# Performance work log

Measured on AMD Instinct MI355X. Metric: run time of the kernel, lower is better.

The kernel has to match this reference:

```python
import jax, jax.numpy as jnp
import numpy as np

N = 8192          # total samples = n_ways * num_instances
D = 512           # embedding dim
NUM_INSTANCES = 8 # shots per class
MARGIN = 0.3
W = 1.0
EPS = 1e-12


def setup_inputs() -> dict:
    key = jax.random.key(0)
    inputs = jax.random.normal(key, (N, D), dtype=jnp.float32)
    # targets[i] = class id; classes are contiguous blocks of NUM_INSTANCES
    targets = jnp.arange(N, dtype=jnp.int32) // NUM_INSTANCES
    return {"inputs": inputs, "targets": targets}


def _pairwise_euclid(a, b):
    # sqrt(clamp(||a||^2 + ||b||^2 - 2 a.b, eps)) -- same as torch addmm path
    sq_a = jnp.sum(a * a, axis=1)          # [na]
    sq_b = jnp.sum(b * b, axis=1)          # [nb]
    d2 = sq_a[:, None] + sq_b[None, :] - 2.0 * (a @ b.T)
    return jnp.sqrt(jnp.clip(d2, EPS, None))


def reference(inputs, targets):
    n = inputs.shape[0]
    n_ways = n // NUM_INSTANCES

    dist = _pairwise_euclid(inputs, inputs)              # [n, n]
    mask = targets[:, None] == targets[None, :]          # same-class mask

    # batch-hard mining: hardest positive (max same-class dist),
    # hardest negative (min different-class dist), fully vectorized
    dist_ap = jnp.max(jnp.where(mask, dist, -jnp.inf), axis=1)  # [n]
    dist_an = jnp.min(jnp.where(mask, jnp.inf, dist), axis=1)   # [n]

    # MarginRankingLoss with y=1: mean(relu(-(dist_an - dist_ap) + margin))
    loss = jnp.mean(jax.nn.relu(dist_ap - dist_an + MARGIN))

    dist_p = jnp.mean(dist_ap)
    dist_n = jnp.mean(dist_an)

    # prototype accuracy
    protos = inputs.reshape(n_ways, NUM_INSTANCES, -1).mean(axis=1)  # [n_ways, D]
    logits = _pairwise_euclid(inputs, protos)                        # [n, n_ways]
    estimate = jnp.argmin(logits, axis=1)
    labels = jnp.arange(n_ways, dtype=estimate.dtype).repeat(NUM_INSTANCES)
    acc = jnp.mean((estimate == labels).astype(jnp.float32))

    return (W * loss, acc, dist_p, dist_n)
```

## Files before the change

### kernel.cpp

```cpp
#include <hip/hip_runtime.h>
#include <hip/hip_bf16.h>
#include <stdint.h>

#define NTOT  8192
#define DIM   512
#define NI    8
#define NWAYS 1024
#define TILE  128
#define BK    64
#define NSYM  2080
#define NBLK  2592
#define MARGINV 0.3f

typedef float f32x4 __attribute__((ext_vector_type(4)));

__device__ __forceinline__ unsigned f2o(float f) {
  unsigned u = __float_as_uint(f);
  return (u & 0x80000000u) ? ~u : (u | 0x80000000u);
}
__device__ __forceinline__ float o2f(unsigned u) {
  u = (u & 0x80000000u) ? (u & 0x7fffffffu) : ~u;
  return __uint_as_float(u);
}

__device__ __forceinline__ float wave_sum64(float v) {
#pragma unroll
  for (int s = 32; s; s >>= 1) v += __shfl_xor(v, s, 64);
  return v;
}

__device__ __forceinline__ void async_ld16(const void* g, void* l) {
  __builtin_amdgcn_global_load_lds(
      (__attribute__((address_space(1))) void*)(uintptr_t)g,
      (__attribute__((address_space(3))) void*)l, 16, 0, 0);
}

__global__ __launch_bounds__(256) void prep(
    const float* __restrict__ A, float* __restrict__ sq,
    float* __restrict__ psq, unsigned char* __restrict__ A8,
    unsigned char* __restrict__ P8,
    unsigned* __restrict__ an_u32, unsigned* __restrict__ ap_u32,
    unsigned long long* __restrict__ pr_key) {
  const int w = threadIdx.x >> 6;
  const int l = threadIdx.x & 63;
  const int b = blockIdx.x;
  if (b < NTOT / 4) {
    const int row = b * 4 + w;
    const float4* rp = (const float4*)(A + (size_t)row * DIM);
    unsigned* op = (unsigned*)(A8 + (size_t)row * DIM);
    float s = 0.f;
#pragma unroll
    for (int m = 0; m < 2; ++m) {
      const float4 v = rp[l + 64 * m];
      s = fmaf(v.x, v.x, fmaf(v.y, v.y, fmaf(v.z, v.z, fmaf(v.w, v.w, s))));
      int wd = 0;
      wd = __builtin_amdgcn_cvt_pk_fp8_f32(v.x, v.y, wd, false);
      wd = __builtin_amdgcn_cvt_pk_fp8_f32(v.z, v.w, wd, true);
      op[l + 64 * m] = (unsigned)wd;
    }
    s = wave_sum64(s);
    if (l == 0) {
      sq[row] = s;
      an_u32[row] = ~0u;
      ap_u32[row] = 0u;
      pr_key[row] = ~0ull;
    }
  } else {
    const int c = (b - NTOT / 4) * 4 + w;
    unsigned* op = (unsigned*)(P8 + (size_t)c * DIM);
    float s = 0.f;
#pragma unroll
    for (int m = 0; m < 2; ++m) {
      float4 p = {0.f, 0.f, 0.f, 0.f};
#pragma unroll
      for (int r = 0; r < NI; ++r) {
        const float4 v =
            ((const float4*)(A + (size_t)(c * NI + r) * DIM))[l + 64 * m];
        p.x += v.x; p.y += v.y; p.z += v.z; p.w += v.w;
      }
      p.x *= (1.f / NI); p.y *= (1.f / NI); p.z *= (1.f / NI); p.w *= (1.f / NI);
      s = fmaf(p.x, p.x, fmaf(p.y, p.y, fmaf(p.z, p.z, fmaf(p.w, p.w, s))));
      int wd = 0;
      wd = __builtin_amdgcn_cvt_pk_fp8_f32(p.x, p.y, wd, false);
      wd = __builtin_amdgcn_cvt_pk_fp8_f32(p.z, p.w, wd, true);
      op[l + 64 * m] = (unsigned)wd;
    }
    s = wave_sum64(s);
    if (l == 0) psq[c] = s;
  }
}

__global__ __launch_bounds__(256) void gemm_fused(
    const unsigned char* __restrict__ A, const unsigned char* __restrict__ P,
    const float* __restrict__ sq, const float* __restrict__ psq,
    unsigned* __restrict__ an_u32, unsigned* __restrict__ ap_u32,
    unsigned long long* __restrict__ pr_key) {
  __shared__ __align__(16) unsigned char As[2][TILE * BK];
  __shared__ __align__(16) unsigned char Bs[2][TILE * BK];
  __shared__ unsigned rmin[TILE];
  __shared__ unsigned cmin[TILE];
  __shared__ unsigned amax[TILE];
  __shared__ unsigned long long rowkey[TILE][2];

  const int braw = blockIdx.x;
  const int b = (braw & 7) * (NBLK / 8) + (braw >> 3);
  const bool isProto = b >= NSYM;
  int bi, bj;
  const unsigned char* Bmat;
  const float* sqB;
  if (!isProto) {
    int rem = b, Si = 0, Sj = 0;
    for (;;) {
      const int cnt = (Si == Sj) ? 36 : 64;
      if (rem < cnt) break;
      rem -= cnt;
      ++Si;
      if (Si > Sj) { Si = 0; ++Sj; }
    }
    int bi_l, bj_l;
    if (Si == Sj) {
      bj_l = 0;
      while ((bj_l + 1) * (bj_l + 2) / 2 <= rem) ++bj_l;
      bi_l = rem - bj_l * (bj_l + 1) / 2;
    } else {
      bi_l = rem & 7;
      bj_l = rem >> 3;
    }
    bi = Si * 8 + bi_l;
    bj = Sj * 8 + bj_l;
    Bmat = A;
    sqB = sq;
  } else {
    const int p = b - NSYM;
    bj = p & 7;
    bi = p >> 3;
    Bmat = P;
    sqB = psq;
  }
  const int rowBase = bi * TILE;
  const int colBase = bj * TILE;
  const bool isDiag = !isProto && (bi == bj);
  const bool colSide = !isProto && (bi != bj);

  const int t = threadIdx.x;
  const int lane = t & 63;
  const int wv = t >> 6;
  const int wr = wv >> 1;
  const int wc = wv & 1;
  const int quad = lane >> 4;
  const int lc = lane & 15;

  if (t < TILE) { rmin[t] = ~0u; cmin[t] = ~0u; amax[t] = 0u; }

  const int kf = (lc ^ (lc >> 2)) & 3;
  int koff[2];
#pragma unroll
  for (int c = 0; c < 2; ++c)
    koff[c] = (((c * 2 + (quad >> 1)) ^ kf) * 16) + (quad & 1) * 8;

  int rowA[4], rowB[4];
#pragma unroll
  for (int x = 0; x < 4; ++x) {
    rowA[x] = (wr * 64 + x * 16 + lc) * BK;
    rowB[x] = (wc * 64 + x * 16 + lc) * BK;
  }

  const int l4 = lane >> 2;
  const int ul = ((lane & 3) ^ ((l4 ^ (l4 >> 2)) & 3)) * 16;
  const unsigned char* gA = A + (size_t)(rowBase + l4) * DIM + ul;
  const unsigned char* gB = Bmat + (size_t)(colBase + l4) * DIM + ul;
  const int ldsL = lane * 16;

  f32x4 acc[4][4] = {};

#pragma unroll
  for (int j = 0; j < 2; ++j) {
    const int rr = wv * 2 + j;
    async_ld16(gA + (size_t)rr * 16 * DIM, &As[0][rr * 1024 + ldsL]);
    async_ld16(gB + (size_t)rr * 16 * DIM, &Bs[0][rr * 1024 + ldsL]);
  }
  __syncthreads();

#pragma unroll
  for (int it = 0; it < 8; ++it) {
    const int cur = it & 1;
    const int nxt = cur ^ 1;
    const int kt = it * BK;
    if (it < 7) {
#pragma unroll
      for (int j = 0; j < 2; ++j) {
        const int rr = wv * 2 + j;
        async_ld16(gA + (size_t)rr * 16 * DIM + kt + BK, &As[nxt][rr * 1024 + ldsL]);
        async_ld16(gB + (size_t)rr * 16 * DIM + kt + BK, &Bs[nxt][rr * 1024 + ldsL]);
      }
    }
    const unsigned char* Ac = &As[cur][0];
    const unsigned char* Bc = &Bs[cur][0];
#pragma unroll
    for (int c = 0; c < 2; ++c) {
      long af[4], bfr[4];
#pragma unroll
      for (int x = 0; x < 4; ++x) {
        af[x]  = *(const long*)(Ac + rowA[x] + koff[c]);
        bfr[x] = *(const long*)(Bc + rowB[x] + koff[c]);
      }
#pragma unroll
      for (int x = 0; x < 4; ++x)
#pragma unroll
        for (int y = 0; y < 4; ++y)
          acc[x][y] = __builtin_amdgcn_mfma_f32_16x16x32_fp8_fp8(
              af[x], bfr[y], acc[x][y], 0, 0, 0);
    }
    __syncthreads();
  }

  float sb[4];
#pragma unroll
  for (int y = 0; y < 4; ++y) sb[y] = sqB[colBase + wc * 64 + y * 16 + lc];

  const float INF = __int_as_float(0x7f800000);

  if (!isProto) {
#pragma unroll
    for (int x = 0; x < 4; ++x) {
#pragma unroll
      for (int r = 0; r < 4; ++r) {
        const int row = rowBase + wr * 64 + x * 16 + quad * 4 + r;
        float mv = INF, mx = -INF;
#pragma unroll
        for (int y = 0; y < 4; ++y) {
          const float v = fmaf(-2.f, acc[x][y][r], sb[y]);
          if (isDiag) {
            const int col = colBase + wc * 64 + y * 16 + lc;
            const bool same = (row >> 3) == (col >> 3);
            mv = fminf(mv, same ? INF : v);
            mx = fmaxf(mx, same ? v : -INF);
          } else {
            mv = fminf(mv, v);
          }
        }
#pragma unroll
        for (int s = 1; s < 16; s <<= 1) {
          mv = fminf(mv, __shfl_xor(mv, s, 64));
          if (isDiag) mx = fmaxf(mx, __shfl_xor(mx, s, 64));
        }
        if (lc == 0) {
          atomicMin(&rmin[row - rowBase], f2o(mv));
          if (isDiag) atomicMax(&amax[row - rowBase], f2o(mx));
        }
      }
    }
    if (colSide) {
      float sa[4][4];
#pragma unroll
      for (int x = 0; x < 4; ++x)
#pragma unroll
        for (int r = 0; r < 4; ++r)
          sa[x][r] = sq[rowBase + wr * 64 + x * 16 + quad * 4 + r];
#pragma unroll
      for (int y = 0; y < 4; ++y) {
        float cv = INF;
#pragma unroll
        for (int x = 0; x < 4; ++x)
#pragma unroll
          for (int r = 0; r < 4; ++r)
            cv = fminf(cv, fmaf(-2.f, acc[x][y][r], sa[x][r]));
        cv = fminf(cv, __shfl_xor(cv, 16, 64));
        cv = fminf(cv, __shfl_xor(cv, 32, 64));
        if (quad == 0) atomicMin(&cmin[wc * 64 + y * 16 + lc], f2o(cv));
      }
    }
  } else {
#pragma unroll
    for (int x = 0; x < 4; ++x) {
      unsigned long long kmin[4] = {~0ull, ~0ull, ~0ull, ~0ull};
#pragma unroll
      for (int y = 0; y < 4; ++y) {
        const int col = colBase + wc * 64 + y * 16 + lc;
#pragma unroll
        for (int r = 0; r < 4; ++r) {
          const float v = fmaf(-2.f, acc[x][y][r], sb[y]);
          const unsigned long long kn =
              ((unsigned long long)f2o(v) << 32) | (unsigned)col;
          if (kn < kmin[r]) kmin[r] = kn;
        }
      }
#pragma unroll
      for (int r = 0; r < 4; ++r) {
#pragma unroll
        for (int s = 1; s < 16; s <<= 1) {
          const unsigned long long o = __shfl_xor(kmin[r], s, 64);
          if (o < kmin[r]) kmin[r] = o;
        }
      }
      if (lc == 0) {
#pragma unroll
        for (int r = 0; r < 4; ++r)
          rowkey[wr * 64 + x * 16 + quad * 4 + r][wc] = kmin[r];
      }
    }
  }

  __syncthreads();
  if (isProto) {
    if (t < TILE) {
      unsigned long long a = rowkey[t][0];
      const unsigned long long c = rowkey[t][1];
      if (c < a) a = c;
      atomicMin(pr_key + rowBase + t, a);
    }
  } else {
    if (t < TILE) {
      atomicMin(an_u32 + rowBase + t, rmin[t]);
    } else if (t < 2 * TILE) {
      const int i = t - TILE;
      if (colSide) atomicMin(an_u32 + colBase + i, cmin[i]);
      else if (isDiag) atomicMax(ap_u32 + rowBase + i, amax[i]);
    }
  }
}

__global__ void finalize_kernel(const float* __restrict__ sq,
                                const unsigned* __restrict__ an_u32,
                                const unsigned* __restrict__ ap_u32,
                                const unsigned long long* __restrict__ pr_key,
                                float* __restrict__ out) {
  const int tid = threadIdx.x;
  float loss = 0.f, sp = 0.f, sn = 0.f, acc = 0.f;
#pragma unroll
  for (int i = tid; i < NTOT; i += 1024) {
    const float s = sq[i];
    const float ap = sqrtf(fmaxf(s + o2f(ap_u32[i]), 1e-12f));
    const float an = sqrtf(fmaxf(s + o2f(an_u32[i]), 1e-12f));
    loss += fmaxf(ap - an + MARGINV, 0.f);
    sp += ap;
    sn += an;
    acc += ((unsigned)(pr_key[i] & 0xffffffffu) == (unsigned)(i >> 3)) ? 1.f : 0.f;
  }
  loss = wave_sum64(loss);
  sp = wave_sum64(sp);
  sn = wave_sum64(sn);
  acc = wave_sum64(acc);
  __shared__ float red[16][4];
  const int w = tid >> 6, l = tid & 63;
  if (l == 0) { red[w][0] = loss; red[w][1] = acc; red[w][2] = sp; red[w][3] = sn; }
  __syncthreads();
  if (tid == 0) {
    float L = 0, Ac = 0, Pm = 0, Nn = 0;
    for (int i = 0; i < 16; ++i) {
      L += red[i][0]; Ac += red[i][1]; Pm += red[i][2]; Nn += red[i][3];
    }
    out[0] = L / NTOT;
    out[1] = Ac / NTOT;
    out[2] = Pm / NTOT;
    out[3] = Nn / NTOT;
  }
}

extern "C" void kernel_launch(void* const* d_in, const int* in_sizes, int n_in,
                              void* d_out, int out_size, void* d_ws, size_t ws_size,
                              hipStream_t stream) {
  const float* inputs = (const float*)d_in[0];
  float* out = (float*)d_out;
  char* w = (char*)d_ws;
  float* sq  = (float*)(w);
  float* psq = (float*)(w + 32768);
  unsigned* an_u32 = (unsigned*)(w + 36864);
  unsigned* ap_u32 = (unsigned*)(w + 69632);
  unsigned long long* pr_key = (unsigned long long*)(w + 102400);
  unsigned char* A8 = (unsigned char*)(w + 167936);
  unsigned char* P8 = (unsigned char*)(w + 167936 + (size_t)NTOT * DIM);

  prep<<<NTOT / 4 + NWAYS / 4, 256, 0, stream>>>(inputs, sq, psq, A8, P8,
                                                 an_u32, ap_u32, pr_key);
  gemm_fused<<<NBLK, 256, 0, stream>>>(A8, P8, sq, psq,
                                       an_u32, ap_u32, pr_key);
  finalize_kernel<<<1, 1024, 0, stream>>>(sq, an_u32, ap_u32, pr_key, out);
}
```

Baseline: 149.4 us.

## Triple-buffer LDS tiles with vmcnt-based waits, hoist norm loads, raise MFMA priority

Replaces the double-buffered async global-to-LDS pipeline with a three-stage ring that prefetches two K-tiles ahead. It uses explicit s_waitcnt vmcnt plus s_barrier in place of __syncthreads, so one barrier per iteration covers both load completion and buffer reuse. The squared-norm loads for the epilogue are hoisted before the main loop so their latency overlaps the GEMM, and s_setprio raises wave priority around the MFMA bursts. The third buffer adds LDS per block, which may reduce occupancy. The hand-counted vmcnt values assume the hoisted sq loads retire early and that the issue order stays as written.

```diff
diff --git a/kernel.cpp b/kernel.cpp
--- a/kernel.cpp
+++ b/kernel.cpp
@@ -8,11 +8,15 @@
 #define NWAYS 1024
 #define TILE  128
 #define BK    64
+#define NBUF  3
 #define NSYM  2080
 #define NBLK  2592
 #define MARGINV 0.3f
 
 typedef float f32x4 __attribute__((ext_vector_type(4)));
+
+#define VMWAIT_BAR(N) \
+  asm volatile("s_waitcnt vmcnt(" #N ")\n\ts_barrier" ::: "memory")
 
 __device__ __forceinline__ unsigned f2o(float f) {
   unsigned u = __float_as_uint(f);
@@ -95,8 +99,8 @@
     const float* __restrict__ sq, const float* __restrict__ psq,
     unsigned* __restrict__ an_u32, unsigned* __restrict__ ap_u32,
     unsigned long long* __restrict__ pr_key) {
-  __shared__ __align__(16) unsigned char As[2][TILE * BK];
-  __shared__ __align__(16) unsigned char Bs[2][TILE * BK];
+  __shared__ __align__(16) unsigned char As[NBUF][TILE * BK];
+  __shared__ __align__(16) unsigned char Bs[NBUF][TILE * BK];
   __shared__ unsigned rmin[TILE];
   __shared__ unsigned cmin[TILE];
   __shared__ unsigned amax[TILE];
@@ -152,6 +156,19 @@
 
   if (t < TILE) { rmin[t] = ~0u; cmin[t] = ~0u; amax[t] = 0u; }
 
+  float sb[4];
+#pragma unroll
+  for (int y = 0; y < 4; ++y) sb[y] = sqB[colBase + wc * 64 + y * 16 + lc];
+  float sa[4][4];
+  if (colSide) {
+#pragma unroll
+    for (int x = 0; x < 4; ++x)
+#pragma unroll
+      for (int r = 0; r < 4; ++r)
+        sa[x][r] = sq[rowBase + wr * 64 + x * 16 + quad * 4 + r];
+  }
+  asm volatile("" ::: "memory");
+
   const int kf = (lc ^ (lc >> 2)) & 3;
   int koff[2];
 #pragma unroll
@@ -174,28 +191,31 @@
   f32x4 acc[4][4] = {};
 
 #pragma unroll
-  for (int j = 0; j < 2; ++j) {
-    const int rr = wv * 2 + j;
-    async_ld16(gA + (size_t)rr * 16 * DIM, &As[0][rr * 1024 + ldsL]);
-    async_ld16(gB + (size_t)rr * 16 * DIM, &Bs[0][rr * 1024 + ldsL]);
-  }
-  __syncthreads();
+  for (int tt = 0; tt < 2; ++tt) {
+#pragma unroll
+    for (int j = 0; j < 2; ++j) {
+      const int rr = wv * 2 + j;
+      async_ld16(gA + (size_t)rr * 16 * DIM + tt * BK, &As[tt][rr * 1024 + ldsL]);
+      async_ld16(gB + (size_t)rr * 16 * DIM + tt * BK, &Bs[tt][rr * 1024 + ldsL]);
+    }
+  }
 
 #pragma unroll
   for (int it = 0; it < 8; ++it) {
-    const int cur = it & 1;
-    const int nxt = cur ^ 1;
-    const int kt = it * BK;
-    if (it < 7) {
+    if (it < 7) VMWAIT_BAR(4);
+    else       VMWAIT_BAR(0);
+    if (it < 6) {
+      const int nb = (it + 2) % NBUF;
+      const int kt2 = (it + 2) * BK;
 #pragma unroll
       for (int j = 0; j < 2; ++j) {
         const int rr = wv * 2 + j;
-        async_ld16(gA + (size_t)rr * 16 * DIM + kt + BK, &As[nxt][rr * 1024 + ldsL]);
-        async_ld16(gB + (size_t)rr * 16 * DIM + kt + BK, &Bs[nxt][rr * 1024 + ldsL]);
-      }
-    }
-    const unsigned char* Ac = &As[cur][0];
-    const unsigned char* Bc = &Bs[cur][0];
+        async_ld16(gA + (size_t)rr * 16 * DIM + kt2, &As[nb][rr * 1024 + ldsL]);
+        async_ld16(gB + (size_t)rr * 16 * DIM + kt2, &Bs[nb][rr * 1024 + ldsL]);
+      }
+    }
+    const unsigned char* Ac = &As[it % NBUF][0];
+    const unsigned char* Bc = &Bs[it % NBUF][0];
 #pragma unroll
     for (int c = 0; c < 2; ++c) {
       long af[4], bfr[4];
@@ -204,19 +224,16 @@
         af[x]  = *(const long*)(Ac + rowA[x] + koff[c]);
         bfr[x] = *(const long*)(Bc + rowB[x] + koff[c]);
       }
+      __builtin_amdgcn_s_setprio(1);
 #pragma unroll
       for (int x = 0; x < 4; ++x)
 #pragma unroll
         for (int y = 0; y < 4; ++y)
           acc[x][y] = __builtin_amdgcn_mfma_f32_16x16x32_fp8_fp8(
               af[x], bfr[y], acc[x][y], 0, 0, 0);
-    }
-    __syncthreads();
-  }
-
-  float sb[4];
-#pragma unroll
-  for (int y = 0; y < 4; ++y) sb[y] = sqB[colBase + wc * 64 + y * 16 + lc];
+      __builtin_amdgcn_s_setprio(0);
+    }
+  }
 
   const float INF = __int_as_float(0x7f800000);
 
@@ -251,12 +268,6 @@
       }
     }
     if (colSide) {
-      float sa[4][4];
-#pragma unroll
-      for (int x = 0; x < 4; ++x)
-#pragma unroll
-        for (int r = 0; r < 4; ++r)
-          sa[x][r] = sq[rowBase + wr * 64 + x * 16 + quad * 4 + r];
 #pragma unroll
       for (int y = 0; y < 4; ++y) {
         float cv = INF;
```

Measured after the change: 147.0 us. Within noise of the previous version (-1.6%).
